# Optimization experiments

Measured on AMD Instinct MI355X. Metric: run time of the kernel, lower is better.

The kernel has to match this reference:

```python
import jax, jax.numpy as jnp
import numpy as np

N = 20000   # nodes
E = 320000  # edges
H = 4       # attention heads
GAT_SLOPE = 0.2   # DGL GATv2Conv internal leaky_relu slope
ACT_SLOPE = 0.01  # nn.LeakyReLU default slope


def gatv2_layer(h, src, dst, Wl, Wr, attn, b):
    """DGL GATv2Conv (share_weights=False, bias=True, eval mode).
    h: [N, Fin]; Wl/Wr: [Fin, H*D]; attn: [H, D]; b: [H*D]. Returns [N, H, D]."""
    n = h.shape[0]
    Hh, D = attn.shape
    fs = (h @ Wl).reshape(n, Hh, D)  # source projection
    fd = (h @ Wr).reshape(n, Hh, D)  # destination projection
    # edge-wise GATv2 score: a^T leaky_relu(Wl h_u + Wr h_v)
    e = jax.nn.leaky_relu(fs[src] + fd[dst], negative_slope=GAT_SLOPE)  # [E,H,D]
    logit = jnp.einsum('ehd,hd->eh', e, attn)  # [E,H]
    # edge softmax over incoming edges of each dst node (numerically stable)
    m = jax.ops.segment_max(logit, dst, num_segments=n)
    a = jnp.exp(logit - m[dst])
    s = jax.ops.segment_sum(a, dst, num_segments=n)
    alpha = a / s[dst]  # [E,H]
    out = jax.ops.segment_sum(alpha[:, :, None] * fs[src], dst, num_segments=n)
    return out + b.reshape(1, Hh, D)


def setup_inputs() -> dict:
    key = jax.random.key(0)
    ks = jax.random.split(key, 16)

    def w(k, shape, fan_in):
        return (jax.random.normal(k, shape, jnp.float32) / np.float32(np.sqrt(fan_in)))

    return {
        'n_feat': jax.random.normal(ks[0], (N, 512), jnp.float32),
        'src': jax.random.randint(ks[1], (E,), 0, N, jnp.int32),
        'dst': jax.random.randint(ks[2], (E,), 0, N, jnp.int32),
        # layer 0: 512 -> H x 128
        'Wl0': w(ks[3], (512, H * 128), 512), 'Wr0': w(ks[4], (512, H * 128), 512),
        'attn0': w(ks[5], (H, 128), 128), 'b0': jnp.zeros((H * 128,), jnp.float32),
        # layer 1: 128 -> H x 128
        'Wl1': w(ks[6], (128, H * 128), 128), 'Wr1': w(ks[7], (128, H * 128), 128),
        'attn1': w(ks[8], (H, 128), 128), 'b1': jnp.zeros((H * 128,), jnp.float32),
        # layer 2 (output): 128 -> H x 64
        'Wl2': w(ks[9], (128, H * 64), 128), 'Wr2': w(ks[10], (128, H * 64), 128),
        'attn2': w(ks[11], (H, 64), 64), 'b2': jnp.zeros((H * 64,), jnp.float32),
    }


def reference(n_feat, src, dst, Wl0, Wr0, attn0, b0, Wl1, Wr1, attn1, b1,
              Wl2, Wr2, attn2, b2):
    h = n_feat.reshape(n_feat.shape[0], -1)  # nn.Flatten
    for (Wl, Wr, attn, b) in ((Wl0, Wr0, attn0, b0),
                              (Wl1, Wr1, attn1, b1),
                              (Wl2, Wr2, attn2, b2)):
        h = gatv2_layer(h, src, dst, Wl, Wr, attn, b)  # [N,H,D]
        h = h.mean(axis=1)                              # head mean
        h = jax.nn.leaky_relu(h, negative_slope=ACT_SLOPE)
    # dgl.mean_nodes: per-graph mean readout (single graph -> [1, out])
    return h.mean(axis=0, keepdims=True)
```

## Files before the change

### kernel.cpp

```cpp
#include <hip/hip_runtime.h>
#include <hip/hip_bf16.h>
#include <stdint.h>


#define GAT_SLOPE 0.2f
#define ACT_SLOPE 0.01f

typedef _Float16 half8 __attribute__((ext_vector_type(8)));
typedef _Float16 v2h __attribute__((ext_vector_type(2)));
typedef float floatx4 __attribute__((ext_vector_type(4)));

struct TransDesc {
  const float* src;
  _Float16* dst;
  int K, M, off;
};
struct PreArgs {
  TransDesc d[6];
  int wTotal;
  const float* nf;
  _Float16* A0;
  int aTotal;
  const int* dst;
  int* counts;
  int E;
};

__global__ __launch_bounds__(256) void preproc_kernel(PreArgs pa) {
  int i = blockIdx.x * 256 + threadIdx.x;
  const int total = pa.wTotal + pa.aTotal + pa.E;
  if (i >= total) return;
  if (i < pa.wTotal) {
    int q = 0;
#pragma unroll
    for (int j = 1; j < 6; ++j)
      if (i >= pa.d[j].off) q = j;
    int local = i - pa.d[q].off;
    int K = pa.d[q].K, M = pa.d[q].M;
    int k = local / M, m = local % M;
    pa.d[q].dst[(size_t)m * K + k] = (_Float16)pa.d[q].src[local];
  } else if (i < pa.wTotal + pa.aTotal) {
    int j = i - pa.wTotal;
    pa.A0[j] = (_Float16)pa.nf[j];
  } else {
    int e = i - pa.wTotal - pa.aTotal;
    atomicAdd(&pa.counts[pa.dst[e]], 1);
  }
}

__device__ __forceinline__ void gload_lds16(const _Float16* g, _Float16* l) {
  __builtin_amdgcn_global_load_lds(
      (__attribute__((address_space(1))) unsigned int*)g,
      (__attribute__((address_space(3))) unsigned int*)l, 16, 0, 0);
}

#define TM 128
#define TN 128
#define TK 32

__global__ __launch_bounds__(256) void gemm_mfma_dual_kernel(
    const _Float16* __restrict__ A, const _Float16* __restrict__ B0,
    const _Float16* __restrict__ B1, _Float16* __restrict__ C0,
    _Float16* __restrict__ C1, int Nrow, int K, int M, int nStrips,
    int nbxLog2) {
  const int id = blockIdx.x;
  const int xcd = id & 7;
  const int s = id >> 3;
  const int nbx = 1 << nbxLog2;
  const int col = s & (nbx - 1);
  const int chunk = s >> nbxLog2;
  const int strip = chunk * 8 + xcd;
  if (strip >= nStrips) return;

  const int nb = nbx >> 1;
  const bool second = col >= nb;
  const _Float16* B = second ? B1 : B0;
  _Float16* C = second ? C1 : C0;
  const int bn = (second ? col - nb : col) * TN;
  const int bm = strip * TM;

  __shared__ __align__(16) _Float16 As[TM * TK];
  __shared__ __align__(16) _Float16 Bs[TN * TK];

  const int tid = threadIdx.x;
  const int w = tid >> 6;
  const int lane = tid & 63;
  const int wr = w >> 1;
  const int wc = w & 1;
  const int quad = lane >> 4;
  const int lr = lane & 15;

  const int lrow = lane >> 2;
  const int loff = (lane & 3) * 8;

  floatx4 acc[4][4];
#pragma unroll
  for (int i = 0; i < 4; ++i)
#pragma unroll
    for (int j = 0; j < 4; ++j) acc[i][j] = (floatx4){0.f, 0.f, 0.f, 0.f};

  const int KT = K / TK;
  for (int kt = 0; kt < KT; ++kt) {
    const int k0 = kt * TK;
#pragma unroll
    for (int half = 0; half < 2; ++half) {
      const int r0 = w * 32 + half * 16;
      int ga = bm + r0 + lrow;
      if (ga >= Nrow) ga = Nrow - 1;
      gload_lds16(A + (size_t)ga * K + k0 + loff, As + r0 * TK);
      gload_lds16(B + (size_t)(bn + r0 + lrow) * K + k0 + loff, Bs + r0 * TK);
    }
    __syncthreads();

    half8 ar[4], br[4];
#pragma unroll
    for (int i = 0; i < 4; ++i) {
      int row = wr * 64 + i * 16 + lr;
      ar[i] = *(const half8*)(As + row * TK + quad * 8);
    }
#pragma unroll
    for (int j = 0; j < 4; ++j) {
      int colr = wc * 64 + j * 16 + lr;
      br[j] = *(const half8*)(Bs + colr * TK + quad * 8);
    }
#pragma unroll
    for (int i = 0; i < 4; ++i)
#pragma unroll
      for (int j = 0; j < 4; ++j)
        acc[i][j] = __builtin_amdgcn_mfma_f32_16x16x32_f16(ar[i], br[j],
                                                           acc[i][j], 0, 0, 0);
    __syncthreads();
  }

#pragma unroll
  for (int i = 0; i < 4; ++i) {
#pragma unroll
    for (int r = 0; r < 4; ++r) {
      int row = bm + wr * 64 + i * 16 + quad * 4 + r;
      if (row >= Nrow) continue;
#pragma unroll
      for (int j = 0; j < 4; ++j) {
        int colc = bn + wc * 64 + j * 16 + lr;
        C[(size_t)row * M + colc] = (_Float16)acc[i][j][r];
      }
    }
  }
}

__global__ __launch_bounds__(256) void scan_kernel(
    const int* __restrict__ counts, int* __restrict__ rowptr,
    int* __restrict__ cursor, int N) {
  __shared__ int sums[256];
  const int t = threadIdx.x;
  const int C = (N + 255) / 256;
  const int lo = t * C;
  const int hi = min(lo + C, N);
  int s = 0;
  for (int i = lo; i < hi; ++i) s += counts[i];
  sums[t] = s;
  __syncthreads();
  for (int off = 1; off < 256; off <<= 1) {
    int v = (t >= off) ? sums[t - off] : 0;
    __syncthreads();
    sums[t] += v;
    __syncthreads();
  }
  int run = (t == 0) ? 0 : sums[t - 1];
  for (int i = lo; i < hi; ++i) {
    rowptr[i] = run;
    cursor[i] = run;
    run += counts[i];
  }
  if (t == 255) rowptr[N] = run;
}

__global__ __launch_bounds__(256) void scatter_kernel(
    const int* __restrict__ src, const int* __restrict__ dst,
    int* __restrict__ cursor, int* __restrict__ csrc, int E) {
  int e = blockIdx.x * 256 + threadIdx.x;
  if (e < E) {
    int p = atomicAdd(&cursor[dst[e]], 1);
    csrc[p] = src[e];
  }
}

template <int D>
__global__ __launch_bounds__(256) void node_attn_kernel(
    const _Float16* __restrict__ fs, const _Float16* __restrict__ fd,
    const int* __restrict__ rowptr, const int* __restrict__ csrc,
    const float* __restrict__ attn, const float* __restrict__ bias,
    float* __restrict__ hout, _Float16* __restrict__ oh, int N) {
  constexpr int HD = 4 * D;
  constexpr int R = HD / 64;
  constexpr int R2 = R / 2;
  typedef _Float16 halfR __attribute__((ext_vector_type(R)));
  union Frag {
    halfR v;
    v2h h[R2];
    _Float16 s[R];
  };
  const int v = blockIdx.x * 4 + (threadIdx.x >> 6);
  if (v >= N) return;
  const int lane = threadIdx.x & 63;

  const v2h slope2 = {(_Float16)GAT_SLOPE, (_Float16)GAT_SLOPE};

  Frag fdv;
  fdv.v = *(const halfR*)(fd + (size_t)v * HD + lane * R);
  v2h ar2[R2];
#pragma unroll
  for (int j = 0; j < R2; ++j) {
    ar2[j][0] = (_Float16)attn[lane * R + 2 * j];
    ar2[j][1] = (_Float16)attn[lane * R + 2 * j + 1];
  }

  float m = -INFINITY, l = 0.f;
  float O[R];
#pragma unroll
  for (int i = 0; i < R; ++i) O[i] = 0.f;

  const int e0 = rowptr[v];
  const int e1 = rowptr[v + 1];
  int k = e0;
  for (; k + 3 < e1; k += 4) {
    const int s0 = csrc[k];
    const int s1 = csrc[k + 1];
    const int s2 = csrc[k + 2];
    const int s3 = csrc[k + 3];
    Frag t0, t1, t2, t3;
    t0.v = *(const halfR*)(fs + (size_t)s0 * HD + lane * R);
    t1.v = *(const halfR*)(fs + (size_t)s1 * HD + lane * R);
    t2.v = *(const halfR*)(fs + (size_t)s2 * HD + lane * R);
    t3.v = *(const halfR*)(fs + (size_t)s3 * HD + lane * R);
    float p0 = 0.f, p1 = 0.f, p2 = 0.f, p3 = 0.f;
#pragma unroll
    for (int j = 0; j < R2; ++j) {
      v2h x0 = t0.h[j] + fdv.h[j];
      v2h x1 = t1.h[j] + fdv.h[j];
      v2h x2 = t2.h[j] + fdv.h[j];
      v2h x3 = t3.h[j] + fdv.h[j];
      x0 = __builtin_elementwise_max(x0, x0 * slope2);
      x1 = __builtin_elementwise_max(x1, x1 * slope2);
      x2 = __builtin_elementwise_max(x2, x2 * slope2);
      x3 = __builtin_elementwise_max(x3, x3 * slope2);
      p0 = __builtin_amdgcn_fdot2(ar2[j], x0, p0, false);
      p1 = __builtin_amdgcn_fdot2(ar2[j], x1, p1, false);
      p2 = __builtin_amdgcn_fdot2(ar2[j], x2, p2, false);
      p3 = __builtin_amdgcn_fdot2(ar2[j], x3, p3, false);
    }
#pragma unroll
    for (int off = 1; off <= 8; off <<= 1) {
      p0 += __shfl_xor(p0, off, 64);
      p1 += __shfl_xor(p1, off, 64);
      p2 += __shfl_xor(p2, off, 64);
      p3 += __shfl_xor(p3, off, 64);
    }
    const float mq = fmaxf(fmaxf(p0, p1), fmaxf(p2, p3));
    const float w0 = __expf(p0 - mq);
    const float w1 = __expf(p1 - mq);
    const float w2 = __expf(p2 - mq);
    const float w3 = __expf(p3 - mq);
    const float mnew = fmaxf(m, mq);
    const float sc = __expf(m - mnew);
    const float sq = __expf(mq - mnew);
    l = l * sc + (w0 + w1 + w2 + w3) * sq;
#pragma unroll
    for (int i = 0; i < R; ++i) {
      float acc = (float)t0.s[i] * w0;
      acc = fmaf((float)t1.s[i], w1, acc);
      acc = fmaf((float)t2.s[i], w2, acc);
      acc = fmaf((float)t3.s[i], w3, acc);
      O[i] = fmaf(O[i], sc, sq * acc);
    }
    m = mnew;
  }
  for (; k < e1; ++k) {
    const int s0 = csrc[k];
    Frag t0;
    t0.v = *(const halfR*)(fs + (size_t)s0 * HD + lane * R);
    float p0 = 0.f;
#pragma unroll
    for (int j = 0; j < R2; ++j) {
      v2h x0 = t0.h[j] + fdv.h[j];
      x0 = __builtin_elementwise_max(x0, x0 * slope2);
      p0 = __builtin_amdgcn_fdot2(ar2[j], x0, p0, false);
    }
#pragma unroll
    for (int off = 1; off <= 8; off <<= 1) p0 += __shfl_xor(p0, off, 64);
    const float mnew = fmaxf(m, p0);
    const float sc = __expf(m - mnew);
    const float p = __expf(p0 - mnew);
    l = l * sc + p;
#pragma unroll
    for (int i = 0; i < R; ++i)
      O[i] = fmaf(O[i], sc, p * (float)t0.s[i]);
    m = mnew;
  }

  const float inv = (l > 0.f) ? 1.f / l : 0.f;
#pragma unroll
  for (int i = 0; i < R; ++i) O[i] = O[i] * inv + bias[lane * R + i];
#pragma unroll
  for (int i = 0; i < R; ++i) {
    O[i] += __shfl_xor(O[i], 16, 64);
    O[i] += __shfl_xor(O[i], 32, 64);
    float x = O[i] * 0.25f;
    O[i] = x > 0.f ? x : x * ACT_SLOPE;
  }
  if (lane < 16) {
    const size_t base = (size_t)v * D + lane * R;
    if (hout) {
#pragma unroll
      for (int i = 0; i < R; ++i) hout[base + i] = O[i];
    }
    if (oh) {
#pragma unroll
      for (int i = 0; i < R; ++i) oh[base + i] = (_Float16)O[i];
    }
  }
}

__global__ __launch_bounds__(64) void final_mean_kernel(
    const float* __restrict__ h, float* __restrict__ out, int N) {
  const int d = threadIdx.x;
  float acc = 0.f;
  for (int n = blockIdx.x; n < N; n += gridDim.x) acc += h[(size_t)n * 64 + d];
  atomicAdd(&out[d], acc / (float)N);
}

extern "C" void kernel_launch(void* const* d_in, const int* in_sizes, int n_in,
                              void* d_out, int out_size, void* d_ws,
                              size_t ws_size, hipStream_t stream) {
  const float* n_feat = (const float*)d_in[0];
  const int* src = (const int*)d_in[1];
  const int* dst = (const int*)d_in[2];
  const float* Wl[3] = {(const float*)d_in[3], (const float*)d_in[7],
                        (const float*)d_in[11]};
  const float* Wr[3] = {(const float*)d_in[4], (const float*)d_in[8],
                        (const float*)d_in[12]};
  const float* attn[3] = {(const float*)d_in[5], (const float*)d_in[9],
                          (const float*)d_in[13]};
  const float* bias[3] = {(const float*)d_in[6], (const float*)d_in[10],
                          (const float*)d_in[14]};

  const int N = in_sizes[0] / 512;
  const int E = in_sizes[1];
  const int Kdim[3] = {512, 128, 128};
  const int Mdim[3] = {512, 512, 256};

  char* ws = (char*)d_ws;
  size_t o = 0;
  auto alloc = [&](size_t bytes) {
    void* p = ws + o;
    o += (bytes + 15) & ~(size_t)15;
    return p;
  };
  _Float16* fs = (_Float16*)alloc((size_t)N * 512 * 2);
  _Float16* fd = (_Float16*)alloc((size_t)N * 512 * 2);
  _Float16* A0 = (_Float16*)alloc((size_t)N * 512 * 2);
  _Float16* h1 = (_Float16*)alloc((size_t)N * 128 * 2);
  _Float16* h2 = (_Float16*)alloc((size_t)N * 128 * 2);
  float* hfin = (float*)alloc((size_t)N * 64 * 4);
  _Float16 *WlT[3], *WrT[3];
  for (int L = 0; L < 3; ++L) {
    size_t sz = (size_t)Kdim[L] * Mdim[L] * 2;
    WlT[L] = (_Float16*)alloc(sz);
    WrT[L] = (_Float16*)alloc(sz);
  }
  int* counts = (int*)alloc((size_t)N * 4);
  int* rowptr = (int*)alloc((size_t)(N + 1) * 4);
  int* cursor = (int*)alloc((size_t)N * 4);
  int* csrc = (int*)alloc((size_t)E * 4);

  hipMemsetAsync(counts, 0, (size_t)N * sizeof(int), stream);
  {
    PreArgs pa;
    int off = 0;
    for (int L = 0; L < 3; ++L) {
      pa.d[2 * L] = {Wl[L], WlT[L], Kdim[L], Mdim[L], off};
      off += Kdim[L] * Mdim[L];
      pa.d[2 * L + 1] = {Wr[L], WrT[L], Kdim[L], Mdim[L], off};
      off += Kdim[L] * Mdim[L];
    }
    pa.wTotal = off;
    pa.nf = n_feat;
    pa.A0 = A0;
    pa.aTotal = N * 512;
    pa.dst = dst;
    pa.counts = counts;
    pa.E = E;
    int total = pa.wTotal + pa.aTotal + pa.E;
    preproc_kernel<<<(total + 255) / 256, 256, 0, stream>>>(pa);
  }
  scan_kernel<<<1, 256, 0, stream>>>(counts, rowptr, cursor, N);
  scatter_kernel<<<(E + 255) / 256, 256, 0, stream>>>(src, dst, cursor, csrc,
                                                      E);

  const _Float16* Ain[3] = {A0, h1, h2};

  const int nStrips = (N + TM - 1) / TM;
  const int S8 = ((nStrips + 7) / 8) * 8;

  for (int L = 0; L < 3; ++L) {
    const int K = Kdim[L], M = Mdim[L];
    const int nbx = 2 * M / TN;
    const int nbxLog2 = (nbx == 8) ? 3 : 2;
    gemm_mfma_dual_kernel<<<S8 * nbx, 256, 0, stream>>>(
        Ain[L], WlT[L], WrT[L], fs, fd, N, K, M, nStrips, nbxLog2);
    if (L == 0) {
      node_attn_kernel<128><<<(N + 3) / 4, 256, 0, stream>>>(
          fs, fd, rowptr, csrc, attn[L], bias[L], nullptr, h1, N);
    } else if (L == 1) {
      node_attn_kernel<128><<<(N + 3) / 4, 256, 0, stream>>>(
          fs, fd, rowptr, csrc, attn[L], bias[L], nullptr, h2, N);
    } else {
      node_attn_kernel<64><<<(N + 3) / 4, 256, 0, stream>>>(
          fs, fd, rowptr, csrc, attn[L], bias[L], hfin, nullptr, N);
    }
  }

  hipMemsetAsync(d_out, 0, 64 * sizeof(float), stream);
  final_mean_kernel<<<256, 64, 0, stream>>>(hfin, (float*)d_out, N);
}
```

Measured before the change: 412.2 us.

## Split each node's incoming edges across two wavefronts with LDS softmax merge

```diff
diff --git a/kernel.cpp b/kernel.cpp
--- a/kernel.cpp
+++ b/kernel.cpp
@@ -185,7 +185,7 @@
 }
 
 template <int D>
-__global__ __launch_bounds__(256) void node_attn_kernel(
+__global__ __launch_bounds__(128) void node_attn_kernel(
     const _Float16* __restrict__ fs, const _Float16* __restrict__ fd,
     const int* __restrict__ rowptr, const int* __restrict__ csrc,
     const float* __restrict__ attn, const float* __restrict__ bias,
@@ -199,8 +199,9 @@
     v2h h[R2];
     _Float16 s[R];
   };
-  const int v = blockIdx.x * 4 + (threadIdx.x >> 6);
+  const int v = blockIdx.x;
   if (v >= N) return;
+  const int wid = threadIdx.x >> 6;
   const int lane = threadIdx.x & 63;
 
   const v2h slope2 = {(_Float16)GAT_SLOPE, (_Float16)GAT_SLOPE};
@@ -221,8 +222,11 @@
 
   const int e0 = rowptr[v];
   const int e1 = rowptr[v + 1];
-  int k = e0;
-  for (; k + 3 < e1; k += 4) {
+  const int mid = e0 + ((e1 - e0 + 1) >> 1);
+  int k = wid ? mid : e0;
+  const int ke = wid ? e1 : mid;
+
+  for (; k + 3 < ke; k += 4) {
     const int s0 = csrc[k];
     const int s1 = csrc[k + 1];
     const int s2 = csrc[k + 2];
@@ -274,7 +278,7 @@
     }
     m = mnew;
   }
-  for (; k < e1; ++k) {
+  for (; k < ke; ++k) {
     const int s0 = csrc[k];
     Frag t0;
     t0.v = *(const halfR*)(fs + (size_t)s0 * HD + lane * R);
@@ -292,9 +296,30 @@
     const float p = __expf(p0 - mnew);
     l = l * sc + p;
 #pragma unroll
-    for (int i = 0; i < R; ++i)
-      O[i] = fmaf(O[i], sc, p * (float)t0.s[i]);
+    for (int i = 0; i < R; ++i) O[i] = fmaf(O[i], sc, p * (float)t0.s[i]);
     m = mnew;
+  }
+
+  __shared__ float sO[64 * R];
+  __shared__ float sM[64];
+  __shared__ float sL[64];
+  if (wid == 1) {
+    sM[lane] = m;
+    sL[lane] = l;
+#pragma unroll
+    for (int i = 0; i < R; ++i) sO[lane * R + i] = O[i];
+  }
+  __syncthreads();
+  if (wid == 1) return;
+  {
+    const float m1 = sM[lane];
+    const float l1 = sL[lane];
+    const float mstar = fmaxf(m, m1);
+    const float a0 = (l > 0.f) ? __expf(m - mstar) : 0.f;
+    const float a1 = (l1 > 0.f) ? __expf(m1 - mstar) : 0.f;
+    l = l * a0 + l1 * a1;
+#pragma unroll
+    for (int i = 0; i < R; ++i) O[i] = O[i] * a0 + sO[lane * R + i] * a1;
   }
 
   const float inv = (l > 0.f) ? 1.f / l : 0.f;
@@ -408,14 +433,17 @@
     gemm_mfma_dual_kernel<<<S8 * nbx, 256, 0, stream>>>(
         Ain[L], WlT[L], WrT[L], fs, fd, N, K, M, nStrips, nbxLog2);
     if (L == 0) {
-      node_attn_kernel<128><<<(N + 3) / 4, 256, 0, stream>>>(
-          fs, fd, rowptr, csrc, attn[L], bias[L], nullptr, h1, N);
+      node_attn_kernel<128><<<N, 128, 0, stream>>>(fs, fd, rowptr, csrc,
+                                                   attn[L], bias[L], nullptr,
+                                                   h1, N);
     } else if (L == 1) {
-      node_attn_kernel<128><<<(N + 3) / 4, 256, 0, stream>>>(
-          fs, fd, rowptr, csrc, attn[L], bias[L], nullptr, h2, N);
+      node_attn_kernel<128><<<N, 128, 0, stream>>>(fs, fd, rowptr, csrc,
+                                                   attn[L], bias[L], nullptr,
+                                                   h2, N);
     } else {
-      node_attn_kernel<64><<<(N + 3) / 4, 256, 0, stream>>>(
-          fs, fd, rowptr, csrc, attn[L], bias[L], hfin, nullptr, N);
+      node_attn_kernel<64><<<N, 128, 0, stream>>>(fs, fd, rowptr, csrc,
+                                                  attn[L], bias[L], hfin,
+                                                  nullptr, N);
     }
   }
 
```

Result: no change. 415.6 us (+0.8%).
